# Optimization experiments

Measured on AMD Instinct MI355X. Metric: run time of the kernel, lower is better.

Reference implementation:

```python
import jax, jax.numpy as jnp
import numpy as np

N_NODES = 65536
N_GRAPHS = 64


def gcn_conv(x, W, b, src, dst, n):
    # PyG GCNConv: add self-loops, symmetric normalization D^-1/2 (A+I) D^-1/2, then linear.
    xw = x @ W  # [N, F_out]
    deg = jnp.zeros((n,), x.dtype).at[dst].add(1.0) + 1.0  # +1 for self-loop
    dinv = jax.lax.rsqrt(deg)
    norm = dinv[src] * dinv[dst]  # [E]
    agg = jnp.zeros_like(xw).at[dst].add(xw[src] * norm[:, None])
    agg = agg + xw * (dinv * dinv)[:, None]  # self-loop term, norm_ii = 1/deg_i
    return agg + b


def setup_inputs() -> dict:
    key = jax.random.key(0)
    ks = jax.random.split(key, 8)
    E = 524288
    x = jax.random.normal(ks[0], (N_NODES, 1), jnp.float32)
    edge_index = jax.random.randint(ks[1], (2, E), 0, N_NODES, dtype=jnp.int64)
    batch = jnp.sort(jax.random.randint(ks[2], (N_NODES,), 0, N_GRAPHS, dtype=jnp.int64))
    def glorot(k, fi, fo):
        s = np.sqrt(2.0 / (fi + fo)).astype(np.float32)
        return jax.random.normal(k, (fi, fo), jnp.float32) * s
    return {
        "x": x, "edge_index": edge_index, "batch": batch,
        "W1": glorot(ks[3], 1, 128), "b1": jnp.zeros((128,), jnp.float32),
        "W2": glorot(ks[4], 128, 64), "b2": jnp.zeros((64,), jnp.float32),
        "W3": glorot(ks[5], 64, 32), "b3": jnp.zeros((32,), jnp.float32),
        "Wfc": glorot(ks[6], 32, 10), "bfc": jnp.zeros((10,), jnp.float32),
    }


def reference(x, edge_index, batch, W1, b1, W2, b2, W3, b3, Wfc, bfc):
    src, dst = edge_index[0], edge_index[1]
    n = x.shape[0]
    h = jax.nn.relu(gcn_conv(x, W1, b1, src, dst, n))
    # dropout is identity in eval mode
    h = jax.nn.relu(gcn_conv(h, W2, b2, src, dst, n))
    h = jax.nn.relu(gcn_conv(h, W3, b3, src, dst, n))
    # global mean pool per graph
    sums = jax.ops.segment_sum(h, batch, num_segments=N_GRAPHS)  # [B, 32]
    cnts = jax.ops.segment_sum(jnp.ones((n,), h.dtype), batch, num_segments=N_GRAPHS)
    pooled = sums / jnp.maximum(cnts, 1.0)[:, None]
    return pooled @ Wfc + bfc  # [B, 10]
```

## Files before the change

### kernel.cpp

```cpp
#include <hip/hip_runtime.h>
#include <hip/hip_fp16.h>

#define THREADS 256

typedef union { uint2 u; __half2 h[2]; } H4;


__global__ void k_count(const int* __restrict__ dst, int* __restrict__ counts,
                        int* __restrict__ seq, int E) {
    int t = blockIdx.x * blockDim.x + threadIdx.x;
    if (t < E) seq[t] = atomicAdd(&counts[dst[t]], 1);
}

__global__ void k_scan1(const int* __restrict__ counts, const float* __restrict__ x,
                        float* __restrict__ dinv, float* __restrict__ s1,
                        int* __restrict__ rowstart, int* __restrict__ blocksums) {
    __shared__ int s[256];
    int i = blockIdx.x * 256 + threadIdx.x;
    int c = counts[i];
    float d = rsqrtf((float)c + 1.0f);
    dinv[i] = d;
    s1[i] = x[i] * d;
    s[threadIdx.x] = c;
    __syncthreads();
    for (int off = 1; off < 256; off <<= 1) {
        int v = (threadIdx.x >= off) ? s[threadIdx.x - off] : 0;
        __syncthreads();
        s[threadIdx.x] += v;
        __syncthreads();
    }
    rowstart[i] = s[threadIdx.x] - c;
    if (threadIdx.x == 255) blocksums[blockIdx.x] = s[255];
}

__global__ void k_scan3(int* __restrict__ rowstart, const int* __restrict__ blocksums) {
    __shared__ int s[256];
    int c = blocksums[threadIdx.x];
    s[threadIdx.x] = c;
    __syncthreads();
    for (int off = 1; off < 256; off <<= 1) {
        int v = (threadIdx.x >= off) ? s[threadIdx.x - off] : 0;
        __syncthreads();
        s[threadIdx.x] += v;
        __syncthreads();
    }
    int addv = s[blockIdx.x] - blocksums[blockIdx.x];
    int i = blockIdx.x * 256 + threadIdx.x;
    rowstart[i] += addv;
}

__global__ void k_fill(const int* __restrict__ src, const int* __restrict__ dst,
                       const int* __restrict__ rowstart, const int* __restrict__ seq,
                       int* __restrict__ esrc, int E) {
    int e = blockIdx.x * blockDim.x + threadIdx.x;
    if (e >= E) return;
    esrc[rowstart[dst[e]] + seq[e]] = src[e];
}

__global__ void k_tsum(const int* __restrict__ rowstart, const int* __restrict__ counts,
                       const int* __restrict__ esrc, const float* __restrict__ s1,
                       float* __restrict__ t, int N) {
    int i = blockIdx.x * blockDim.x + threadIdx.x;
    if (i >= N) return;
    float acc = s1[i];
    int s0 = rowstart[i], cnt = counts[i];
    for (int p = s0; p < s0 + cnt; ++p) acc += s1[esrc[p]];
    t[i] = acc;
}

#define L12_R 8
__global__ void k_l1l2(const float* __restrict__ t, const float* __restrict__ dinv,
                       const float* __restrict__ W1, const float* __restrict__ b1,
                       const float* __restrict__ W2, __half* __restrict__ xws2, int N) {
    __shared__ float wb[128 * 2];
    __shared__ float W2s[128 * 64];
    for (int idx = threadIdx.x; idx < 128; idx += 256) {
        wb[idx * 2] = W1[idx];
        wb[idx * 2 + 1] = b1[idx];
    }
    for (int idx = threadIdx.x; idx < 128 * 64 / 4; idx += 256)
        reinterpret_cast<float4*>(W2s)[idx] = reinterpret_cast<const float4*>(W2)[idx];
    __syncthreads();

    int c4 = threadIdx.x & 15;
    int rg = threadIdx.x >> 4;
    int base = blockIdx.x * (16 * L12_R) + rg * L12_R;

    float a[L12_R];
#pragma unroll
    for (int r = 0; r < L12_R; ++r) {
        int i = base + r;
        a[r] = (i < N) ? dinv[i] * t[i] : 0.f;
    }
    float4 acc[L12_R] = {};
    for (int k = 0; k < 128; ++k) {
        float2 w1b1 = *reinterpret_cast<const float2*>(&wb[k * 2]);
        float4 w2 = *reinterpret_cast<const float4*>(&W2s[k * 64 + c4 * 4]);
#pragma unroll
        for (int r = 0; r < L12_R; ++r) {
            float h = fmaxf(fmaf(a[r], w1b1.x, w1b1.y), 0.f);
            acc[r].x = fmaf(h, w2.x, acc[r].x);
            acc[r].y = fmaf(h, w2.y, acc[r].y);
            acc[r].z = fmaf(h, w2.z, acc[r].z);
            acc[r].w = fmaf(h, w2.w, acc[r].w);
        }
    }
#pragma unroll
    for (int r = 0; r < L12_R; ++r) {
        int i = base + r;
        if (i < N) {
            float di = dinv[i];
            H4 o;
            o.h[0] = __floats2half2_rn(acc[r].x * di, acc[r].y * di);
            o.h[1] = __floats2half2_rn(acc[r].z * di, acc[r].w * di);
            reinterpret_cast<uint2*>(xws2)[(size_t)i * 16 + c4] = o.u;
        }
    }
}

__global__ void k_l2l3(const int* __restrict__ rowstart, const int* __restrict__ counts,
                       const int* __restrict__ esrc, const __half* __restrict__ xws2,
                       const float* __restrict__ dinv, const float* __restrict__ b2,
                       const float* __restrict__ W3, __half* __restrict__ xws3, int N) {
    __shared__ float W3s[64 * 32];
    __shared__ float h2s[16][64];
    __shared__ float b2s[64];
    for (int idx = threadIdx.x; idx < 64 * 32 / 4; idx += 256)
        reinterpret_cast<float4*>(W3s)[idx] = reinterpret_cast<const float4*>(W3)[idx];
    if (threadIdx.x < 64) b2s[threadIdx.x] = b2[threadIdx.x];
    __syncthreads();

    {
        int c4 = threadIdx.x & 15;
        int r  = threadIdx.x >> 4;
        int i  = blockIdx.x * 16 + r;
        if (i < N) {
            const uint2* x2 = reinterpret_cast<const uint2*>(xws2);
            H4 p; p.u = x2[(size_t)i * 16 + c4];
            float2 f0 = __half22float2(p.h[0]), f1 = __half22float2(p.h[1]);
            float4 acc = {f0.x, f0.y, f1.x, f1.y};
            int s0 = rowstart[i], cnt = counts[i];
            for (int q = s0; q < s0 + cnt; ++q) {
                int s = esrc[q];
                p.u = x2[(size_t)s * 16 + c4];
                f0 = __half22float2(p.h[0]); f1 = __half22float2(p.h[1]);
                acc.x += f0.x; acc.y += f0.y; acc.z += f1.x; acc.w += f1.y;
            }
            float di = dinv[i];
            float4 bv = *reinterpret_cast<const float4*>(&b2s[c4 * 4]);
            float4 h;
            h.x = fmaxf(fmaf(di, acc.x, bv.x), 0.f);
            h.y = fmaxf(fmaf(di, acc.y, bv.y), 0.f);
            h.z = fmaxf(fmaf(di, acc.z, bv.z), 0.f);
            h.w = fmaxf(fmaf(di, acc.w, bv.w), 0.f);
            *reinterpret_cast<float4*>(&h2s[r][c4 * 4]) = h;
        }
    }
    __syncthreads();
    {
        int c  = threadIdx.x & 15;
        int r2 = threadIdx.x >> 4;
        int i2 = blockIdx.x * 16 + r2;
        if (i2 >= N) return;
        float acc0 = 0.f, acc1 = 0.f;
#pragma unroll
        for (int k = 0; k < 64; ++k) {
            float h = h2s[r2][k];
            float2 w = *reinterpret_cast<const float2*>(&W3s[k * 32 + 2 * c]);
            acc0 = fmaf(h, w.x, acc0);
            acc1 = fmaf(h, w.y, acc1);
        }
        float di = dinv[i2];
        reinterpret_cast<__half2*>(xws3)[(size_t)i2 * 16 + c] =
            __floats2half2_rn(acc0 * di, acc1 * di);
    }
}

__global__ void k_l3pool(const int* __restrict__ rowstart, const int* __restrict__ counts,
                         const int* __restrict__ esrc, const __half* __restrict__ xws3,
                         const float* __restrict__ dinv, const float* __restrict__ b3,
                         const int* __restrict__ batch, float* __restrict__ sums,
                         float* __restrict__ cnt, int N) {
    __shared__ float sl[64 * 32];
    __shared__ float cl[64];
    for (int idx = threadIdx.x; idx < 64 * 32; idx += 256) sl[idx] = 0.f;
    if (threadIdx.x < 64) cl[threadIdx.x] = 0.f;
    __syncthreads();

    int c4 = threadIdx.x & 7;
    int r  = threadIdx.x >> 3;
    int i  = blockIdx.x * 32 + r;
    if (i < N) {
        const uint2* x2 = reinterpret_cast<const uint2*>(xws3);
        H4 p; p.u = x2[(size_t)i * 8 + c4];
        float2 f0 = __half22float2(p.h[0]), f1 = __half22float2(p.h[1]);
        float4 acc = {f0.x, f0.y, f1.x, f1.y};
        int s0 = rowstart[i], cc = counts[i];
        for (int q = s0; q < s0 + cc; ++q) {
            int s = esrc[q];
            p.u = x2[(size_t)s * 8 + c4];
            f0 = __half22float2(p.h[0]); f1 = __half22float2(p.h[1]);
            acc.x += f0.x; acc.y += f0.y; acc.z += f1.x; acc.w += f1.y;
        }
        float di = dinv[i];
        const float4 bv = reinterpret_cast<const float4*>(b3)[c4];
        int g = batch[i];
        atomicAdd(&sl[g * 32 + c4 * 4 + 0], fmaxf(fmaf(di, acc.x, bv.x), 0.f));
        atomicAdd(&sl[g * 32 + c4 * 4 + 1], fmaxf(fmaf(di, acc.y, bv.y), 0.f));
        atomicAdd(&sl[g * 32 + c4 * 4 + 2], fmaxf(fmaf(di, acc.z, bv.z), 0.f));
        atomicAdd(&sl[g * 32 + c4 * 4 + 3], fmaxf(fmaf(di, acc.w, bv.w), 0.f));
        if (c4 == 0) atomicAdd(&cl[g], 1.f);
    }
    __syncthreads();

    int start = blockIdx.x * 32;
    if (start >= N) return;
    int g0 = batch[start];
    int g1 = batch[min(start + 31, N - 1)];
    int ng = g1 - g0 + 1;
    for (int idx = threadIdx.x; idx < ng * 32; idx += 256) {
        float v = sl[(g0 + idx / 32) * 32 + (idx & 31)];
        if (v != 0.f) atomicAdd(&sums[(g0 + idx / 32) * 32 + (idx & 31)], v);
    }
    for (int idx = threadIdx.x; idx < ng; idx += 256) {
        float v = cl[g0 + idx];
        if (v != 0.f) atomicAdd(&cnt[g0 + idx], v);
    }
}

__global__ void k_fc(const float* __restrict__ sums, const float* __restrict__ cnt,
                     const float* __restrict__ Wfc, const float* __restrict__ bfc,
                     float* __restrict__ out) {
    int t = blockIdx.x * blockDim.x + threadIdx.x;
    if (t >= 64 * 10) return;
    int g = t / 10, o = t % 10;
    float inv = 1.0f / fmaxf(cnt[g], 1.0f);
    float acc = bfc[o];
#pragma unroll
    for (int f = 0; f < 32; ++f) acc = fmaf(sums[g * 32 + f] * inv, Wfc[f * 10 + o], acc);
    out[t] = acc;
}

extern "C" void kernel_launch(void* const* d_in, const int* in_sizes, int n_in,
                              void* d_out, int out_size, void* d_ws, size_t ws_size,
                              hipStream_t stream) {
    const float* x    = (const float*)d_in[0];
    const int*   ei   = (const int*)d_in[1];
    const int*   batch= (const int*)d_in[2];
    const float* W1   = (const float*)d_in[3];
    const float* b1   = (const float*)d_in[4];
    const float* W2   = (const float*)d_in[5];
    const float* b2   = (const float*)d_in[6];
    const float* W3   = (const float*)d_in[7];
    const float* b3   = (const float*)d_in[8];
    const float* Wfc  = (const float*)d_in[9];
    const float* bfc  = (const float*)d_in[10];
    float* out = (float*)d_out;

    const int N = in_sizes[0];
    const int E = in_sizes[1] / 2;
    const int* src  = ei;
    const int* dstp = ei + E;

    char* ws = (char*)d_ws;
    size_t off = 0;
    auto alloc = [&](size_t bytes) { void* p = ws + off; off = (off + bytes + 15) & ~(size_t)15; return p; };
    int*    counts   = (int*)   alloc((size_t)N * 4);
    int*    rowstart = (int*)   alloc((size_t)N * 4);
    int*    seq      = (int*)   alloc((size_t)E * 4);
    int*    blocksums= (int*)   alloc(256 * 4);
    int*    esrc     = (int*)   alloc((size_t)E * 4);
    float*  dinv     = (float*) alloc((size_t)N * 4);
    float*  s1       = (float*) alloc((size_t)N * 4);
    float*  tsum     = (float*) alloc((size_t)N * 4);
    float*  sums     = (float*) alloc(64 * 32 * 4 + 64 * 4);
    float*  cnt      = sums + 64 * 32;
    __half* xws2     = (__half*)alloc((size_t)N * 64 * 2);
    __half* xws3     = (__half*)alloc((size_t)N * 32 * 2);

    auto blocks = [](long n) { return (int)((n + THREADS - 1) / THREADS); };

    hipMemsetAsync(counts, 0, (size_t)N * 4, stream);
    hipMemsetAsync(sums, 0, (64 * 32 + 64) * 4, stream);

    k_count<<<blocks(E), THREADS, 0, stream>>>(dstp, counts, seq, E);
    k_scan1<<<N / 256, 256, 0, stream>>>(counts, x, dinv, s1, rowstart, blocksums);
    k_scan3<<<N / 256, 256, 0, stream>>>(rowstart, blocksums);
    k_fill <<<blocks(E), THREADS, 0, stream>>>(src, dstp, rowstart, seq, esrc, E);

    k_tsum<<<blocks(N), THREADS, 0, stream>>>(rowstart, counts, esrc, s1, tsum, N);

    k_l1l2<<<(N + 16 * L12_R - 1) / (16 * L12_R), THREADS, 0, stream>>>(tsum, dinv, W1, b1, W2, xws2, N);

    k_l2l3<<<(N + 15) / 16, THREADS, 0, stream>>>(rowstart, counts, esrc, xws2, dinv, b2, W3, xws3, N);

    k_l3pool<<<(N + 31) / 32, THREADS, 0, stream>>>(rowstart, counts, esrc, xws3, dinv, b3, batch, sums, cnt, N);

    k_fc<<<blocks(640), THREADS, 0, stream>>>(sums, cnt, Wfc, bfc, out);
}
```

Measured before the change: 207.7 us.

## Fuse scan fixup, fill, layer-1 sum, and final FC into fewer kernels

Folds the block-offset scan into the fill kernel, where each block rescans the 256 block sums redundantly. The layer-1 neighbour sum moves into the fill step as per-edge float atomics on t, replacing the separate CSR gather kernel. The final FC runs in the last pooling block, found with a global ticket counter, and the two memsets are merged into one contiguous zeroing. This cuts four launches and one pass over the edges, at the cost of atomic contention on t and float-atomic ordering nondeterminism in layer 1.

```diff
diff --git a/kernel.cpp b/kernel.cpp
--- a/kernel.cpp
+++ b/kernel.cpp
@@ -14,13 +14,16 @@
 
 __global__ void k_scan1(const int* __restrict__ counts, const float* __restrict__ x,
                         float* __restrict__ dinv, float* __restrict__ s1,
-                        int* __restrict__ rowstart, int* __restrict__ blocksums) {
+                        float* __restrict__ t, int* __restrict__ rowloc,
+                        int* __restrict__ blocksums) {
     __shared__ int s[256];
     int i = blockIdx.x * 256 + threadIdx.x;
     int c = counts[i];
     float d = rsqrtf((float)c + 1.0f);
     dinv[i] = d;
-    s1[i] = x[i] * d;
+    float sv = x[i] * d;
+    s1[i] = sv;
+    t[i] = sv;
     s[threadIdx.x] = c;
     __syncthreads();
     for (int off = 1; off < 256; off <<= 1) {
@@ -29,43 +32,41 @@
         s[threadIdx.x] += v;
         __syncthreads();
     }
-    rowstart[i] = s[threadIdx.x] - c;
+    rowloc[i] = s[threadIdx.x] - c;
     if (threadIdx.x == 255) blocksums[blockIdx.x] = s[255];
 }
 
-__global__ void k_scan3(int* __restrict__ rowstart, const int* __restrict__ blocksums) {
-    __shared__ int s[256];
-    int c = blocksums[threadIdx.x];
-    s[threadIdx.x] = c;
-    __syncthreads();
-    for (int off = 1; off < 256; off <<= 1) {
-        int v = (threadIdx.x >= off) ? s[threadIdx.x - off] : 0;
+__global__ void k_fill(const int* __restrict__ src, const int* __restrict__ dst,
+                       const int* __restrict__ rowloc, const int* __restrict__ seq,
+                       const int* __restrict__ blocksums, const float* __restrict__ s1,
+                       int* __restrict__ esrc, float* __restrict__ t,
+                       int* __restrict__ rowstart, int E) {
+    __shared__ int boff[256];
+    {
+        int c = blocksums[threadIdx.x];
+        boff[threadIdx.x] = c;
         __syncthreads();
-        s[threadIdx.x] += v;
+        for (int off = 1; off < 256; off <<= 1) {
+            int v = (threadIdx.x >= off) ? boff[threadIdx.x - off] : 0;
+            __syncthreads();
+            boff[threadIdx.x] += v;
+            __syncthreads();
+        }
+        boff[threadIdx.x] -= c;
         __syncthreads();
     }
-    int addv = s[blockIdx.x] - blocksums[blockIdx.x];
-    int i = blockIdx.x * 256 + threadIdx.x;
-    rowstart[i] += addv;
-}
-
-__global__ void k_fill(const int* __restrict__ src, const int* __restrict__ dst,
-                       const int* __restrict__ rowstart, const int* __restrict__ seq,
-                       int* __restrict__ esrc, int E) {
     int e = blockIdx.x * blockDim.x + threadIdx.x;
-    if (e >= E) return;
-    esrc[rowstart[dst[e]] + seq[e]] = src[e];
-}
-
-__global__ void k_tsum(const int* __restrict__ rowstart, const int* __restrict__ counts,
-                       const int* __restrict__ esrc, const float* __restrict__ s1,
-                       float* __restrict__ t, int N) {
-    int i = blockIdx.x * blockDim.x + threadIdx.x;
-    if (i >= N) return;
-    float acc = s1[i];
-    int s0 = rowstart[i], cnt = counts[i];
-    for (int p = s0; p < s0 + cnt; ++p) acc += s1[esrc[p]];
-    t[i] = acc;
+    if (e < E) {
+        int d = dst[e];
+        int sg = src[e];
+        int p = rowloc[d] + boff[d >> 8] + seq[e];
+        esrc[p] = sg;
+        atomicAdd(&t[d], s1[sg]);
+    }
+    if (blockIdx.x < 256) {
+        int i = blockIdx.x * 256 + threadIdx.x;
+        rowstart[i] = rowloc[i] + boff[blockIdx.x];
+    }
 }
 
 #define L12_R 8
@@ -180,9 +181,12 @@
                          const int* __restrict__ esrc, const __half* __restrict__ xws3,
                          const float* __restrict__ dinv, const float* __restrict__ b3,
                          const int* __restrict__ batch, float* __restrict__ sums,
-                         float* __restrict__ cnt, int N) {
+                         float* __restrict__ cnt, int* __restrict__ ticket,
+                         const float* __restrict__ Wfc, const float* __restrict__ bfc,
+                         float* __restrict__ out, int N, int nblocks) {
     __shared__ float sl[64 * 32];
     __shared__ float cl[64];
+    __shared__ int lastflag;
     for (int idx = threadIdx.x; idx < 64 * 32; idx += 256) sl[idx] = 0.f;
     if (threadIdx.x < 64) cl[threadIdx.x] = 0.f;
     __syncthreads();
@@ -214,31 +218,39 @@
     __syncthreads();
 
     int start = blockIdx.x * 32;
-    if (start >= N) return;
-    int g0 = batch[start];
-    int g1 = batch[min(start + 31, N - 1)];
-    int ng = g1 - g0 + 1;
-    for (int idx = threadIdx.x; idx < ng * 32; idx += 256) {
-        float v = sl[(g0 + idx / 32) * 32 + (idx & 31)];
-        if (v != 0.f) atomicAdd(&sums[(g0 + idx / 32) * 32 + (idx & 31)], v);
-    }
-    for (int idx = threadIdx.x; idx < ng; idx += 256) {
-        float v = cl[g0 + idx];
-        if (v != 0.f) atomicAdd(&cnt[g0 + idx], v);
-    }
-}
-
-__global__ void k_fc(const float* __restrict__ sums, const float* __restrict__ cnt,
-                     const float* __restrict__ Wfc, const float* __restrict__ bfc,
-                     float* __restrict__ out) {
-    int t = blockIdx.x * blockDim.x + threadIdx.x;
-    if (t >= 64 * 10) return;
-    int g = t / 10, o = t % 10;
-    float inv = 1.0f / fmaxf(cnt[g], 1.0f);
-    float acc = bfc[o];
-#pragma unroll
-    for (int f = 0; f < 32; ++f) acc = fmaf(sums[g * 32 + f] * inv, Wfc[f * 10 + o], acc);
-    out[t] = acc;
+    if (start < N) {
+        int g0 = batch[start];
+        int g1 = batch[min(start + 31, N - 1)];
+        int ng = g1 - g0 + 1;
+        for (int idx = threadIdx.x; idx < ng * 32; idx += 256) {
+            float v = sl[(g0 + idx / 32) * 32 + (idx & 31)];
+            if (v != 0.f) atomicAdd(&sums[(g0 + idx / 32) * 32 + (idx & 31)], v);
+        }
+        for (int idx = threadIdx.x; idx < ng; idx += 256) {
+            float v = cl[g0 + idx];
+            if (v != 0.f) atomicAdd(&cnt[g0 + idx], v);
+        }
+    }
+
+    __threadfence();
+    __syncthreads();
+    if (threadIdx.x == 0) lastflag = (atomicAdd(ticket, 1) == nblocks - 1) ? 1 : 0;
+    __syncthreads();
+    if (!lastflag) return;
+
+    for (int idx = threadIdx.x; idx < 64 * 32; idx += 256)
+        sl[idx] = __hip_atomic_load(&sums[idx], __ATOMIC_RELAXED, __HIP_MEMORY_SCOPE_AGENT);
+    for (int idx = threadIdx.x; idx < 64; idx += 256)
+        cl[idx] = __hip_atomic_load(&cnt[idx], __ATOMIC_RELAXED, __HIP_MEMORY_SCOPE_AGENT);
+    __syncthreads();
+    for (int tix = threadIdx.x; tix < 640; tix += 256) {
+        int g = tix / 10, o = tix % 10;
+        float inv = 1.0f / fmaxf(cl[g], 1.0f);
+        float acc = bfc[o];
+#pragma unroll
+        for (int f = 0; f < 32; ++f) acc = fmaf(sl[g * 32 + f] * inv, Wfc[f * 10 + o], acc);
+        out[tix] = acc;
+    }
 }
 
 extern "C" void kernel_launch(void* const* d_in, const int* in_sizes, int n_in,
@@ -266,6 +278,11 @@
     size_t off = 0;
     auto alloc = [&](size_t bytes) { void* p = ws + off; off = (off + bytes + 15) & ~(size_t)15; return p; };
     int*    counts   = (int*)   alloc((size_t)N * 4);
+    float*  sums     = (float*) alloc(64 * 32 * 4);
+    float*  cnt      = (float*) alloc(64 * 4);
+    int*    ticket   = (int*)   alloc(16);
+    size_t  zbytes   = (size_t)((char*)ticket + 16 - (char*)counts);
+    int*    rowloc   = (int*)   alloc((size_t)N * 4);
     int*    rowstart = (int*)   alloc((size_t)N * 4);
     int*    seq      = (int*)   alloc((size_t)E * 4);
     int*    blocksums= (int*)   alloc(256 * 4);
@@ -273,28 +290,20 @@
     float*  dinv     = (float*) alloc((size_t)N * 4);
     float*  s1       = (float*) alloc((size_t)N * 4);
     float*  tsum     = (float*) alloc((size_t)N * 4);
-    float*  sums     = (float*) alloc(64 * 32 * 4 + 64 * 4);
-    float*  cnt      = sums + 64 * 32;
     __half* xws2     = (__half*)alloc((size_t)N * 64 * 2);
     __half* xws3     = (__half*)alloc((size_t)N * 32 * 2);
 
     auto blocks = [](long n) { return (int)((n + THREADS - 1) / THREADS); };
 
-    hipMemsetAsync(counts, 0, (size_t)N * 4, stream);
-    hipMemsetAsync(sums, 0, (64 * 32 + 64) * 4, stream);
+    hipMemsetAsync(counts, 0, zbytes, stream);
 
     k_count<<<blocks(E), THREADS, 0, stream>>>(dstp, counts, seq, E);
-    k_scan1<<<N / 256, 256, 0, stream>>>(counts, x, dinv, s1, rowstart, blocksums);
-    k_scan3<<<N / 256, 256, 0, stream>>>(rowstart, blocksums);
-    k_fill <<<blocks(E), THREADS, 0, stream>>>(src, dstp, rowstart, seq, esrc, E);
-
-    k_tsum<<<blocks(N), THREADS, 0, stream>>>(rowstart, counts, esrc, s1, tsum, N);
-
+    k_scan1<<<N / 256, 256, 0, stream>>>(counts, x, dinv, s1, tsum, rowloc, blocksums);
+    k_fill <<<blocks(E), THREADS, 0, stream>>>(src, dstp, rowloc, seq, blocksums, s1,
+                                               esrc, tsum, rowstart, E);
     k_l1l2<<<(N + 16 * L12_R - 1) / (16 * L12_R), THREADS, 0, stream>>>(tsum, dinv, W1, b1, W2, xws2, N);
-
     k_l2l3<<<(N + 15) / 16, THREADS, 0, stream>>>(rowstart, counts, esrc, xws2, dinv, b2, W3, xws3, N);
-
-    k_l3pool<<<(N + 31) / 32, THREADS, 0, stream>>>(rowstart, counts, esrc, xws3, dinv, b3, batch, sums, cnt, N);
-
-    k_fc<<<blocks(640), THREADS, 0, stream>>>(sums, cnt, Wfc, bfc, out);
-}
+    int npool = (N + 31) / 32;
+    k_l3pool<<<npool, THREADS, 0, stream>>>(rowstart, counts, esrc, xws3, dinv, b3, batch,
+                                            sums, cnt, ticket, Wfc, bfc, out, N, npool);
+}
```

New measurement: 328.3 us. 1.58x slower.
